# Kernel optimization log

Hardware: AMD Instinct MI355X
Metric: run time of the kernel (lower is better)

The kernel has to match this reference:

```python
import jax, jax.numpy as jnp
import numpy as np

NTOK, NINP, NREL = 50257, 512, 200
N, L, EPS = 1024, 64, 32  # n sequences, seq length, edges per sequence
E = N * EPS               # m.sum()


def setup_inputs() -> dict:
    key = jax.random.key(0)
    k1, k2, k3, k4 = jax.random.split(key, 4)
    seq = jax.random.randint(k1, (N, L), 0, NTOK, dtype=jnp.int32)
    m = jnp.full((N,), EPS, dtype=jnp.int32)          # edges per sequence (constant -> static E)
    rel = jax.random.randint(k2, (E,), 0, NREL, dtype=jnp.int32)
    emb = jax.random.normal(k3, (NTOK, NINP), dtype=jnp.float32)          # nn.Embedding weight
    W = 0.01 * jax.random.normal(k4, (NREL, NINP), dtype=jnp.float32)     # nn.Linear weight
    b = jnp.zeros((NREL,), dtype=jnp.float32)                             # nn.Linear bias
    return {"seq": seq, "m": m, "rel": rel, "emb": emb, "W": W, "b": b}


def reference(seq, m, rel, emb, W, b):
    # logit = linear(embedding(seq).sum(1))
    h = emb[seq].sum(axis=1)                    # (N, NINP) gather + segment-sum over tokens
    logit = h @ W.T + b                         # (N, NREL)

    # multi-label mask: mask[i, r] = True iff some edge of sequence i has relation r
    n_seq = m.shape[0]
    idx = jnp.repeat(jnp.arange(n_seq), m, total_repeat_length=rel.shape[0])  # (E,)
    mask = jnp.zeros((n_seq, logit.shape[1]), dtype=bool).at[idx, rel].set(True)

    # sum of logsigmoid on positive labels + log(1+1e-5 - sigmoid) on negatives, / len(seq)
    logp = jnp.sum(jnp.where(mask,
                             jax.nn.log_sigmoid(logit),
                             jnp.log(1.0 + 1e-5 - jax.nn.sigmoid(logit)))) / seq.shape[0]
    acc = jnp.mean(((logit > 0.5) == mask).astype(jnp.float32))
    return logp, acc
```

## Files before the change

kernel.cpp:

```cpp
#include <hip/hip_runtime.h>

#define NINP 512
#define NREL 200
#define LSEQ 64
#define WT_LD 256
#define SPB 4

typedef float vfloat4 __attribute__((ext_vector_type(4)));

__global__ __launch_bounds__(256) void wt_kernel(
    const float* __restrict__ W,
    float* __restrict__ Wt)
{
    const int b = blockIdx.x;
    const int t = threadIdx.x;
    #pragma unroll
    for (int j = 0; j < 2; ++j) {
        const int k = b * 2 + j;
        Wt[k * WT_LD + t] = (t < NREL) ? W[t * NINP + k] : 0.f;
    }
}

__global__ __launch_bounds__(1024) void fused_kernel(
    const int* __restrict__ seq,
    const float* __restrict__ emb,
    const float* __restrict__ Wt,
    const int* __restrict__ rel,
    const float* __restrict__ bias,
    float* __restrict__ out,
    int N, int eps)
{
    __shared__ int    toks[SPB * LSEQ];
    __shared__ vfloat4 hpart[16][2][64];
    __shared__ float  h_pack[NINP][SPB];
    __shared__ float4 pd[16][SPB][64];
    __shared__ unsigned int maskbits[SPB][8];
    __shared__ float  red_lp[16], red_ac[16];

    const int i0   = blockIdx.x * SPB;
    const int t    = threadIdx.x;
    const int wave = t >> 6;
    const int lane = t & 63;

    if (t < SPB * LSEQ) toks[t] = seq[i0 * LSEQ + t];
    if (t < SPB * 8) ((unsigned int*)maskbits)[t] = 0u;
    __syncthreads();

    if (t < SPB * 32) {
        const int s = t >> 5, j = t & 31;
        if (j < eps) {
            int r = rel[(i0 + s) * eps + j];
            atomicOr(&maskbits[s][r >> 5], 1u << (r & 31));
        }
    }

    {
        const int rbase = (wave >> 2) * LSEQ + (wave & 3) * 16;
        vfloat4 lo = (vfloat4)0.f;
        vfloat4 hi = (vfloat4)0.f;
        #pragma unroll
        for (int j0 = 0; j0 < 16; j0 += 8) {
            const vfloat4* rp[8];
            #pragma unroll
            for (int j = 0; j < 8; ++j)
                rp[j] = (const vfloat4*)(emb +
                    (long)__builtin_amdgcn_readfirstlane(toks[rbase + j0 + j]) * NINP);
            vfloat4 l[8], h[8];
            #pragma unroll
            for (int j = 0; j < 8; ++j) {
                l[j] = __builtin_nontemporal_load(rp[j] + lane);
                h[j] = __builtin_nontemporal_load(rp[j] + 64 + lane);
            }
            #pragma unroll
            for (int j = 0; j < 4; ++j) {
                l[j] = l[2*j] + l[2*j+1];
                h[j] = h[2*j] + h[2*j+1];
            }
            lo += (l[0] + l[1]) + (l[2] + l[3]);
            hi += (h[0] + h[1]) + (h[2] + h[3]);
        }
        hpart[wave][0][lane] = lo;
        hpart[wave][1][lane] = hi;
    }
    __syncthreads();

    {
        float2 v;
        #pragma unroll
        for (int d = 0; d < 2; ++d) {
            const int idx = 2 * t + d;
            const int s = idx & 3;
            const int k = idx >> 2;
            const int f = k >> 2, c = k & 3;
            const int half = f >> 6, lf = f & 63;
            float sum = 0.f;
            #pragma unroll
            for (int q = 0; q < 4; ++q)
                sum += ((const float*)&hpart[s * 4 + q][half][lf])[c];
            ((float*)&v)[d] = sum;
        }
        ((float2*)h_pack)[t] = v;
    }
    __syncthreads();

    {
        const float4* Wt4 = (const float4*)Wt;
        float4 a0 = make_float4(0.f, 0.f, 0.f, 0.f);
        float4 a1 = a0, a2 = a0, a3 = a0;
        const int kbase = wave * 32;
        #pragma unroll 4
        for (int k = kbase; k < kbase + 32; ++k) {
            const float4 wv = Wt4[k * 64 + lane];
            const float4 hp = ((const float4*)h_pack)[k];
            a0.x += hp.x * wv.x; a0.y += hp.x * wv.y; a0.z += hp.x * wv.z; a0.w += hp.x * wv.w;
            a1.x += hp.y * wv.x; a1.y += hp.y * wv.y; a1.z += hp.y * wv.z; a1.w += hp.y * wv.w;
            a2.x += hp.z * wv.x; a2.y += hp.z * wv.y; a2.z += hp.z * wv.z; a2.w += hp.z * wv.w;
            a3.x += hp.w * wv.x; a3.y += hp.w * wv.y; a3.z += hp.w * wv.z; a3.w += hp.w * wv.w;
        }
        pd[wave][0][lane] = a0;
        pd[wave][1][lane] = a1;
        pd[wave][2][lane] = a2;
        pd[wave][3][lane] = a3;
    }
    __syncthreads();

    float term = 0.f, match = 0.f;
    {
        const int s = t >> 8;
        const int r = t & 255;
        if (r < NREL) {
            const int f = r >> 2, c = r & 3;
            float dot = bias[r];
            #pragma unroll
            for (int w = 0; w < 16; ++w)
                dot += ((const float*)&pd[w][s][f])[c];
            const unsigned mb = (maskbits[s][r >> 5] >> (r & 31)) & 1u;
            if (mb) {
                term = fminf(dot, 0.f) - log1pf(expf(-fabsf(dot)));
            } else {
                term = logf(1e-5f + 1.f / (1.f + expf(dot)));
            }
            match = (((dot > 0.5f) ? 1u : 0u) == mb) ? 1.f : 0.f;
        }
    }

    #pragma unroll
    for (int off = 32; off > 0; off >>= 1) {
        term  += __shfl_down(term,  off);
        match += __shfl_down(match, off);
    }
    if (lane == 0) { red_lp[wave] = term; red_ac[wave] = match; }
    __syncthreads();
    if (t == 0) {
        float s = 0.f, a = 0.f;
        #pragma unroll
        for (int w = 0; w < 16; ++w) { s += red_lp[w]; a += red_ac[w]; }
        atomicAdd(out + 0, s / (float)N);
        atomicAdd(out + 1, a / ((float)N * (float)NREL));
    }
}

extern "C" void kernel_launch(void* const* d_in, const int* in_sizes, int n_in,
                              void* d_out, int out_size, void* d_ws, size_t ws_size,
                              hipStream_t stream) {
    const int*   seq = (const int*)d_in[0];
    const int*   m   = (const int*)d_in[1]; (void)m;
    const int*   rel = (const int*)d_in[2];
    const float* emb = (const float*)d_in[3];
    const float* W   = (const float*)d_in[4];
    const float* b   = (const float*)d_in[5];
    float* out = (float*)d_out;

    const int N   = in_sizes[1];
    const int eps = in_sizes[2] / N;

    float* Wt = (float*)d_ws;

    hipMemsetAsync(out, 0, 2 * sizeof(float), stream);
    wt_kernel<<<NINP / 2, 256, 0, stream>>>(W, Wt);
    fused_kernel<<<N / SPB, 1024, 0, stream>>>(seq, emb, Wt, rel, b, out, N, eps);
}
```

Before: 170.6 us.

## Remove token staging and a block barrier, tile the W transpose, fold the memset

Token indices are read directly from global memory instead of being staged in shared memory, which removes one block-wide barrier. The h_pack reduction is remapped so each wave produces exactly the slice it consumes in the GEMV, which lets a local LDS waitcnt replace the __syncthreads. The W transpose now goes through a shared-memory tile for coalesced access and also zeroes the output, which drops the separate memset launch. The risks are slightly more scalar global loads for tokens and subtle correctness reliance on the per-wave data ownership.

Result: no change. 172.1 us, median of 2 (+0.9%).

```diff
diff --git a/kernel.cpp b/kernel.cpp
--- a/kernel.cpp
+++ b/kernel.cpp
@@ -5,19 +5,34 @@
 #define LSEQ 64
 #define WT_LD 256
 #define SPB 4
+#define NW 16
 
 typedef float vfloat4 __attribute__((ext_vector_type(4)));
 
 __global__ __launch_bounds__(256) void wt_kernel(
     const float* __restrict__ W,
-    float* __restrict__ Wt)
+    float* __restrict__ Wt,
+    float* __restrict__ out)
 {
-    const int b = blockIdx.x;
-    const int t = threadIdx.x;
+    __shared__ float tile[64][65];
+    const int b  = blockIdx.x;
+    const int br = b >> 3, bk = b & 7;
+    const int r0 = br * 64, k0 = bk * 64;
+    const int t  = threadIdx.x;
+    const int ty = t >> 6, tx = t & 63;
+
+    if (b == 0 && t < 2) out[t] = 0.f;
+
     #pragma unroll
-    for (int j = 0; j < 2; ++j) {
-        const int k = b * 2 + j;
-        Wt[k * WT_LD + t] = (t < NREL) ? W[t * NINP + k] : 0.f;
+    for (int jj = 0; jj < 16; ++jj) {
+        const int i = jj * 4 + ty;
+        tile[i][tx] = (r0 + i < NREL) ? W[(r0 + i) * NINP + k0 + tx] : 0.f;
+    }
+    __syncthreads();
+    #pragma unroll
+    for (int jj = 0; jj < 16; ++jj) {
+        const int k = k0 + jj * 4 + ty;
+        Wt[k * WT_LD + r0 + tx] = tile[tx][jj * 4 + ty];
     }
 }
 
@@ -30,32 +45,22 @@
     float* __restrict__ out,
     int N, int eps)
 {
-    __shared__ int    toks[SPB * LSEQ];
-    __shared__ vfloat4 hpart[16][2][64];
-    __shared__ float  h_pack[NINP][SPB];
-    __shared__ float4 pd[16][SPB][64];
+    __shared__ vfloat4 hpart[NW][2][64];
+    __shared__ float4  h_pack4[NINP];
+    __shared__ float4  pd[NW][SPB][64];
     __shared__ unsigned int maskbits[SPB][8];
-    __shared__ float  red_lp[16], red_ac[16];
+    __shared__ float   red_lp[NW], red_ac[NW];
 
     const int i0   = blockIdx.x * SPB;
     const int t    = threadIdx.x;
-    const int wave = t >> 6;
+    const int wave = __builtin_amdgcn_readfirstlane(t >> 6);
     const int lane = t & 63;
 
-    if (t < SPB * LSEQ) toks[t] = seq[i0 * LSEQ + t];
     if (t < SPB * 8) ((unsigned int*)maskbits)[t] = 0u;
-    __syncthreads();
-
-    if (t < SPB * 32) {
-        const int s = t >> 5, j = t & 31;
-        if (j < eps) {
-            int r = rel[(i0 + s) * eps + j];
-            atomicOr(&maskbits[s][r >> 5], 1u << (r & 31));
-        }
-    }
 
     {
-        const int rbase = (wave >> 2) * LSEQ + (wave & 3) * 16;
+        const int sq = wave >> 2, qq = wave & 3;
+        const int* sp = seq + (long)(i0 + sq) * LSEQ + qq * 16;
         vfloat4 lo = (vfloat4)0.f;
         vfloat4 hi = (vfloat4)0.f;
         #pragma unroll
@@ -64,7 +69,7 @@
             #pragma unroll
             for (int j = 0; j < 8; ++j)
                 rp[j] = (const vfloat4*)(emb +
-                    (long)__builtin_amdgcn_readfirstlane(toks[rbase + j0 + j]) * NINP);
+                    (long)__builtin_amdgcn_readfirstlane(sp[j0 + j]) * NINP);
             vfloat4 l[8], h[8];
             #pragma unroll
             for (int j = 0; j < 8; ++j) {
@@ -84,24 +89,34 @@
     }
     __syncthreads();
 
+    if (t < SPB * 32) {
+        const int s = t >> 5, j = t & 31;
+        if (j < eps) {
+            int r = rel[(i0 + s) * eps + j];
+            atomicOr(&maskbits[s][r >> 5], 1u << (r & 31));
+        }
+    }
+
     {
+        const int kbase = wave * 32;
+        const int p = lane >> 5;
+        const int k = kbase + (lane & 31);
+        const int fg = k >> 2, c = k & 3;
+        const int half = fg >> 6, fl = fg & 63;
         float2 v;
         #pragma unroll
         for (int d = 0; d < 2; ++d) {
-            const int idx = 2 * t + d;
-            const int s = idx & 3;
-            const int k = idx >> 2;
-            const int f = k >> 2, c = k & 3;
-            const int half = f >> 6, lf = f & 63;
+            const int sbar = 2 * p + d;
             float sum = 0.f;
             #pragma unroll
             for (int q = 0; q < 4; ++q)
-                sum += ((const float*)&hpart[s * 4 + q][half][lf])[c];
+                sum += ((const float*)&hpart[sbar * 4 + q][half][fl])[c];
             ((float*)&v)[d] = sum;
         }
-        ((float2*)h_pack)[t] = v;
+        ((float2*)&h_pack4[k])[p] = v;
     }
-    __syncthreads();
+    asm volatile("s_waitcnt lgkmcnt(0)" ::: "memory");
+    __builtin_amdgcn_sched_barrier(0);
 
     {
         const float4* Wt4 = (const float4*)Wt;
@@ -111,7 +126,7 @@
         #pragma unroll 4
         for (int k = kbase; k < kbase + 32; ++k) {
             const float4 wv = Wt4[k * 64 + lane];
-            const float4 hp = ((const float4*)h_pack)[k];
+            const float4 hp = h_pack4[k];
             a0.x += hp.x * wv.x; a0.y += hp.x * wv.y; a0.z += hp.x * wv.z; a0.w += hp.x * wv.w;
             a1.x += hp.y * wv.x; a1.y += hp.y * wv.y; a1.z += hp.y * wv.z; a1.w += hp.y * wv.w;
             a2.x += hp.z * wv.x; a2.y += hp.z * wv.y; a2.z += hp.z * wv.z; a2.w += hp.z * wv.w;
@@ -132,7 +147,7 @@
             const int f = r >> 2, c = r & 3;
             float dot = bias[r];
             #pragma unroll
-            for (int w = 0; w < 16; ++w)
+            for (int w = 0; w < NW; ++w)
                 dot += ((const float*)&pd[w][s][f])[c];
             const unsigned mb = (maskbits[s][r >> 5] >> (r & 31)) & 1u;
             if (mb) {
@@ -154,7 +169,7 @@
     if (t == 0) {
         float s = 0.f, a = 0.f;
         #pragma unroll
-        for (int w = 0; w < 16; ++w) { s += red_lp[w]; a += red_ac[w]; }
+        for (int w = 0; w < NW; ++w) { s += red_lp[w]; a += red_ac[w]; }
         atomicAdd(out + 0, s / (float)N);
         atomicAdd(out + 1, a / ((float)N * (float)NREL));
     }
@@ -176,7 +191,6 @@
 
     float* Wt = (float*)d_ws;
 
-    hipMemsetAsync(out, 0, 2 * sizeof(float), stream);
-    wt_kernel<<<NINP / 2, 256, 0, stream>>>(W, Wt);
+    wt_kernel<<<32, 256, 0, stream>>>(W, Wt, out);
     fused_kernel<<<N / SPB, 1024, 0, stream>>>(seq, emb, Wt, rel, b, out, N, eps);
 }
```
